# Kernel tuning notes

Measured on AMD Instinct MI355X. Metric: run time of the kernel, lower is better.

The kernel has to match this reference:

```python
import jax, jax.numpy as jnp
import numpy as np

K_DEPTH = 3
JAC_A = 1.0  # alpha (Jacobi a)
JAC_B = 1.0  # beta  (Jacobi b)


def jacobi_filter(sig, gammas):
    """Polynomial graph filter g(sigma) = sum_k gamma_k * P_k^{(a,b)}(sigma),
    Jacobi recurrence applied elementwise (Sigma is diagonal spectrum), domain [-1,1],
    fixed inner scalings (fixI=True => alphas=1)."""
    a, b = JAC_A, JAC_B
    xs = [jnp.ones_like(sig)]
    # L = 1
    coef1 = (a - b) / 2.0
    coef2 = (a + b + 2.0) / 2.0
    xs.append(coef1 * xs[0] + coef2 * sig * xs[0])
    for L in range(2, K_DEPTH + 1):
        cl = 2.0 * L * (L + a + b) * (2 * L - 2 + a + b)
        c1 = (2 * L + a + b - 1) * (2 * L + a + b) * (2 * L + a + b - 2)
        c2 = (2 * L + a + b - 1) * (a * a - b * b)
        c3 = 2.0 * (L - 1 + a) * (L - 1 + b) * (2 * L + a + b)
        xs.append((c1 / cl) * sig * xs[-1] - (c2 / cl) * xs[-1] - (c3 / cl) * xs[-2])
    basis = jnp.stack(xs, axis=0)  # [K+1, B, H, L, d]
    return jnp.einsum('k,kbhld->bhld', gammas, basis)


def setup_inputs() -> dict:
    key = jax.random.key(0)
    ks = jax.random.split(key, 7)
    B, L, Ha, Hs, d = 4, 2048, 4, 4, 64
    mk = lambda k, H: jax.random.normal(k, (B, L, H, d), dtype=jnp.float32)
    return {
        'U': mk(ks[0], Ha),
        'Sigma': mk(ks[1], Ha),
        'V': mk(ks[2], Ha),
        'values': mk(ks[3], Ha),
        'queries_softmax': mk(ks[4], Hs),
        'keys_softmax': mk(ks[5], Hs),
        'values_softmax': mk(ks[6], Hs),
        'gammas': jnp.ones((K_DEPTH + 1,), dtype=jnp.float32),
    }


def reference(U, Sigma, V, values, queries_softmax, keys_softmax, values_softmax, gammas):
    d_k = U.shape[-1]
    # ---- AGF (SVD) heads ----
    Uh = jax.nn.softmax(jnp.transpose(U, (0, 2, 1, 3)), axis=-1)        # [B,H,L,d]
    Vt = jax.nn.softmax(jnp.transpose(V, (0, 2, 3, 1)), axis=-1)        # [B,H,d,L]
    vals = jnp.transpose(values, (0, 2, 1, 3))                           # [B,H,L,d]
    sig = jax.nn.sigmoid(jnp.transpose(Sigma, (0, 2, 1, 3)))             # [B,H,L,d]
    gf = jacobi_filter(sig, gammas)                                       # [B,H,L,d]
    kv = jnp.einsum('bhdl,bhle->bhde', Vt, vals)                          # [B,H,d,d]
    out_agf = jnp.einsum('bhld,bhde->bhle', Uh * gf, kv)                  # [B,H,L,d]
    out_agf = jnp.transpose(out_agf, (0, 2, 1, 3))                        # [B,L,H,d]
    # ---- orthogonality loss ----
    eye = jnp.eye(d_k, dtype=Uh.dtype)
    sym_u = jnp.einsum('bhld,bhle->bhde', Uh, Uh) - eye
    sym_v = jnp.einsum('bhdl,bhel->bhde', Vt, Vt) - eye
    ortho_loss = jnp.mean(jnp.abs(sym_u), axis=(1, 2, 3)) + jnp.mean(jnp.abs(sym_v), axis=(1, 2, 3))
    # ---- softmax (flash) heads ----
    q = jnp.transpose(queries_softmax, (0, 2, 1, 3))
    k = jnp.transpose(keys_softmax, (0, 2, 1, 3))
    v = jnp.transpose(values_softmax, (0, 2, 1, 3))
    scores = jnp.einsum('bhld,bhsd->bhls', q, k) / jnp.sqrt(jnp.asarray(d_k, q.dtype))
    attn = jax.nn.softmax(scores, axis=-1)
    out_sm = jnp.einsum('bhls,bhsd->bhld', attn, v)
    out_sm = jnp.transpose(out_sm, (0, 2, 1, 3))                          # [B,L,H,d]
    out = jnp.concatenate([out_agf, out_sm], axis=2)                      # [B,L,2H,d]
    return out, ortho_loss
```

## Files before the change

kernel.cpp:

```cpp
#include <hip/hip_runtime.h>
#include <hip/hip_bf16.h>

#define BB 4
#define SEQ 2048
#define NH 4
#define D 64
#define NPAIR 16
#define HOUT 8
#define LOSS_BASE ((size_t)BB * SEQ * HOUT * D)

#define OFF_PART 0
#define N_PART   (4 * 16 * 3 * 4096)
#define OFF_SPART (OFF_PART + N_PART)
#define N_SPART  (16 * 32 * 64)
#define OFF_LPART (OFF_SPART + N_SPART)
#define N_LPART  (2 * 16 * 2048)
#define OFF_OPART (OFF_LPART + N_LPART)
#define N_OPART  (2 * 16 * 2048 * 64)
#define OFF_US   (OFF_OPART + N_OPART)
#define USZ ((size_t)16 * 2048 * 64)

typedef __attribute__((ext_vector_type(8))) short bf16x8;
typedef __attribute__((ext_vector_type(4))) float f32x4;
typedef __attribute__((ext_vector_type(8))) unsigned short us8;
typedef __attribute__((ext_vector_type(4))) unsigned short us4;

__device__ __forceinline__ unsigned short f2bf(float x) {
    union { float f; unsigned u; } v; v.f = x;
    unsigned r = v.u + 0x7fffu + ((v.u >> 16) & 1u);
    return (unsigned short)(r >> 16);
}
__device__ __forceinline__ float bf2f(unsigned short u) {
    union { unsigned u; float f; } v; v.u = ((unsigned)u) << 16; return v.f;
}
__device__ __forceinline__ void load16(const float* p, float* v) {
    const float4* q = (const float4*)p;
    float4 a = q[0], b = q[1], c = q[2], d = q[3];
    v[0]=a.x; v[1]=a.y; v[2]=a.z; v[3]=a.w;
    v[4]=b.x; v[5]=b.y; v[6]=b.z; v[7]=b.w;
    v[8]=c.x; v[9]=c.y; v[10]=c.z; v[11]=c.w;
    v[12]=d.x; v[13]=d.y; v[14]=d.z; v[15]=d.w;
}
__device__ __forceinline__ void wr_bf16x16(unsigned short* dst, const float* v) {
    us8 w0, w1;
#pragma unroll
    for (int i = 0; i < 8; i++) { w0[i] = f2bf(v[i]); w1[i] = f2bf(v[8 + i]); }
    *(us8*)dst = w0; *(us8*)(dst + 8) = w1;
}

__global__ __launch_bounds__(256) void prep(const float* __restrict__ U, const float* __restrict__ Vagf,
                                            const float* __restrict__ vals, const float* __restrict__ Ksm,
                                            const float* __restrict__ Vsm,
                                            float* __restrict__ ws, unsigned short* __restrict__ usb,
                                            float* __restrict__ out) {
    int lt = blockIdx.x, p = blockIdx.y;
    int b = p >> 2, h = p & 3;
    int tid = threadIdx.x;
    int r = tid >> 2;
    int c4 = tid & 3;
    int c0 = c4 * 16;
    __shared__ float T[64][68];
    unsigned short* Khi   = usb;
    unsigned short* VbfT  = usb + USZ;
    unsigned short* UhT   = usb + 2 * USZ;
    unsigned short* EhiT  = usb + 3 * USZ;
    unsigned short* EloT  = usb + 4 * USZ;
    unsigned short* valsT = usb + 5 * USZ;
    float* Spart = ws + OFF_SPART;

    const size_t gbase = ((size_t)(b * SEQ + lt * 64 + r) * NH + h) * D + c0;
    const size_t tbase = ((size_t)p * 64 + r) * 2048 + lt * 64 + c0;
    float v[16], e[16];

    load16(U + gbase, v);
    float mx = v[0];
#pragma unroll
    for (int k = 1; k < 16; k++) mx = fmaxf(mx, v[k]);
    mx = fmaxf(mx, __shfl_xor(mx, 1));
    mx = fmaxf(mx, __shfl_xor(mx, 2));
    float sm = 0.0f;
#pragma unroll
    for (int k = 0; k < 16; k++) { v[k] = __expf(v[k] - mx); sm += v[k]; }
    sm += __shfl_xor(sm, 1);
    sm += __shfl_xor(sm, 2);
    float inv = 1.0f / sm;
#pragma unroll
    for (int k = 0; k < 16; k++) T[r][c0 + k] = v[k] * inv;
    __syncthreads();
#pragma unroll
    for (int k = 0; k < 16; k++) e[k] = T[c0 + k][r];
    wr_bf16x16(UhT + tbase, e);
    __syncthreads();

    load16(Vagf + gbase, v);
#pragma unroll
    for (int k = 0; k < 16; k++) T[r][c0 + k] = __expf(v[k]);
    __syncthreads();
    float ssum = 0.0f;
#pragma unroll
    for (int k = 0; k < 16; k++) { e[k] = T[c0 + k][r]; ssum += e[k]; }
    ssum += __shfl_xor(ssum, 1);
    ssum += __shfl_xor(ssum, 2);
    if (c4 == 0) Spart[(p * 32 + lt) * 64 + r] = ssum;
    {
        us8 h0, h1, l0, l1;
#pragma unroll
        for (int i = 0; i < 8; i++) {
            unsigned short hh = f2bf(e[i]);
            h0[i] = hh; l0[i] = f2bf(e[i] - bf2f(hh));
            unsigned short h2 = f2bf(e[8 + i]);
            h1[i] = h2; l1[i] = f2bf(e[8 + i] - bf2f(h2));
        }
        *(us8*)(EhiT + tbase) = h0; *(us8*)(EhiT + tbase + 8) = h1;
        *(us8*)(EloT + tbase) = l0; *(us8*)(EloT + tbase + 8) = l1;
    }
    __syncthreads();

    load16(vals + gbase, v);
#pragma unroll
    for (int k = 0; k < 16; k++) T[r][c0 + k] = v[k];
    __syncthreads();
#pragma unroll
    for (int k = 0; k < 16; k++) e[k] = T[c0 + k][r];
    wr_bf16x16(valsT + tbase, e);
    __syncthreads();

    load16(Vsm + gbase, v);
#pragma unroll
    for (int k = 0; k < 16; k++) T[r][c0 + k] = v[k];
    __syncthreads();
#pragma unroll
    for (int k = 0; k < 16; k++) e[k] = T[c0 + k][r];
    wr_bf16x16(VbfT + tbase, e);

    load16(Ksm + gbase, v);
    wr_bf16x16(Khi + ((size_t)(p * SEQ + lt * 64 + r)) * 64 + c0, v);

    if (lt == 0 && p == 0 && tid < BB) out[LOSS_BASE + tid] = 0.0f;
}

__global__ __launch_bounds__(256) void gram(const unsigned short* __restrict__ usb,
                                            float* __restrict__ part) {
    int split = blockIdx.x, p = blockIdx.y;
    int tid = threadIdx.x;
    int w = tid >> 6, lane = tid & 63, lm = lane & 15, quad = lane >> 4;
    const unsigned short* UhT   = usb + 2 * USZ;
    const unsigned short* EhiT  = usb + 3 * USZ;
    const unsigned short* EloT  = usb + 4 * USZ;
    const unsigned short* valsT = usb + 5 * USZ;
    __shared__ __align__(16) unsigned short Ut[64 * 40], Eh[64 * 40], El[64 * 40], Vt[64 * 40];
    f32x4 su[4], sv[4], kv[4];
#pragma unroll
    for (int i = 0; i < 4; i++) { su[i] = (f32x4){0,0,0,0}; sv[i] = (f32x4){0,0,0,0}; kv[i] = (f32x4){0,0,0,0}; }
    int srow = tid >> 2;
    int sseg = (tid & 3) * 8;

    for (int step = 0; step < 16; ++step) {
        int l0 = split * 512 + step * 32;
        __syncthreads();
        size_t gb = ((size_t)p * 64 + srow) * 2048 + l0 + sseg;
        *(us8*)&Ut[srow * 40 + sseg] = *(const us8*)(UhT + gb);
        *(us8*)&Eh[srow * 40 + sseg] = *(const us8*)(EhiT + gb);
        *(us8*)&El[srow * 40 + sseg] = *(const us8*)(EloT + gb);
        *(us8*)&Vt[srow * 40 + sseg] = *(const us8*)(valsT + gb);
        __syncthreads();
        int ao = (w * 16 + lm) * 40 + quad * 8;
        bf16x8 au  = *(const bf16x8*)&Ut[ao];
        bf16x8 aeh = *(const bf16x8*)&Eh[ao];
        bf16x8 ael = *(const bf16x8*)&El[ao];
#pragma unroll
        for (int nt = 0; nt < 4; nt++) {
            int bo = (nt * 16 + lm) * 40 + quad * 8;
            bf16x8 bu  = *(const bf16x8*)&Ut[bo];
            bf16x8 beh = *(const bf16x8*)&Eh[bo];
            bf16x8 bv  = *(const bf16x8*)&Vt[bo];
            su[nt] = __builtin_amdgcn_mfma_f32_16x16x32_bf16(au,  bu,  su[nt], 0, 0, 0);
            sv[nt] = __builtin_amdgcn_mfma_f32_16x16x32_bf16(aeh, beh, sv[nt], 0, 0, 0);
            kv[nt] = __builtin_amdgcn_mfma_f32_16x16x32_bf16(aeh, bv,  kv[nt], 0, 0, 0);
            kv[nt] = __builtin_amdgcn_mfma_f32_16x16x32_bf16(ael, bv,  kv[nt], 0, 0, 0);
        }
    }
    float* dst = part + (size_t)(split * 16 + p) * 3 * 4096;
#pragma unroll
    for (int nt = 0; nt < 4; nt++)
#pragma unroll
        for (int reg = 0; reg < 4; reg++) {
            int off = (w * 16 + quad * 4 + reg) * 64 + nt * 16 + lm;
            dst[off] = su[nt][reg];
            dst[4096 + off] = sv[nt][reg];
            dst[8192 + off] = kv[nt][reg];
        }
}

__global__ __launch_bounds__(256) void agf_ortho(const float* __restrict__ U, const float* __restrict__ Sg,
                                                 const float* __restrict__ gam, const float* __restrict__ part,
                                                 const float* __restrict__ Spart, float* __restrict__ out) {
    int p = blockIdx.y;
    int tid = threadIdx.x;
    __shared__ float cis[64];
    __shared__ float red[4][64];
    {
        int d = tid & 63, grp = tid >> 6;
        float s = 0.0f;
#pragma unroll
        for (int i = 0; i < 8; i++) s += Spart[(p * 32 + grp * 8 + i) * 64 + d];
        red[grp][d] = s;
        __syncthreads();
        if (tid < 64) cis[tid] = 1.0f / (red[0][tid] + red[1][tid] + red[2][tid] + red[3][tid]);
        __syncthreads();
    }
    if (blockIdx.x == 32) {
        float s = 0.0f;
        for (int idx = tid; idx < 8192; idx += 256) {
            int g = idx >> 12, i = idx & 4095;
            float v = 0.0f;
#pragma unroll
            for (int sp = 0; sp < 4; sp++) v += part[((size_t)(sp * 16 + p) * 3 + g) * 4096 + i];
            if (g) v *= cis[i >> 6] * cis[i & 63];
            float dg = ((i >> 6) == (i & 63)) ? 1.0f : 0.0f;
            s += fabsf(v - dg);
        }
#pragma unroll
        for (int o = 32; o > 0; o >>= 1) s += __shfl_xor(s, o);
        __shared__ float r4[4];
        if ((tid & 63) == 0) r4[tid >> 6] = s;
        __syncthreads();
        if (tid == 0) atomicAdd(&out[LOSS_BASE + (p >> 2)], (r4[0] + r4[1] + r4[2] + r4[3]) * (1.0f / 16384.0f));
        return;
    }
    int lt = blockIdx.x;
    int b = p >> 2, h = p & 3;
    __shared__ __align__(16) float kvs[64][68];
    __shared__ __align__(16) float ugs[64][68];
    for (int idx = tid; idx < 4096; idx += 256) {
        float v = 0.0f;
#pragma unroll
        for (int sp = 0; sp < 4; sp++) v += part[((size_t)(sp * 16 + p) * 3 + 2) * 4096 + idx];
        kvs[idx >> 6][idx & 63] = v * cis[idx >> 6];
    }
    {
        int row = tid >> 2;
        int c16 = (tid & 3) * 16;
        size_t ibase = ((size_t)((b * SEQ + lt * 64 + row) * NH + h)) * D + c16;
        float uv[16];
        load16(U + ibase, uv);
        float mx = uv[0];
#pragma unroll
        for (int k = 1; k < 16; k++) mx = fmaxf(mx, uv[k]);
        mx = fmaxf(mx, __shfl_xor(mx, 1));
        mx = fmaxf(mx, __shfl_xor(mx, 2));
        float sm = 0.0f;
#pragma unroll
        for (int k = 0; k < 16; k++) { uv[k] = __expf(uv[k] - mx); sm += uv[k]; }
        sm += __shfl_xor(sm, 1);
        sm += __shfl_xor(sm, 2);
        float inv = 1.0f / sm;
        float sg[16];
        load16(Sg + ibase, sg);
        float g0 = gam[0], g1 = gam[1], g2 = gam[2], g3 = gam[3];
#pragma unroll
        for (int k = 0; k < 16; k++) {
            float sig = 1.0f / (1.0f + __expf(-sg[k]));
            float x1 = 2.0f * sig;
            float x2 = 1.875f * sig * x1 - 0.75f;
            float x3 = 1.8666666666666667f * sig * x2 - 0.8f * x1;
            float gf = g0 + g1 * x1 + g2 * x2 + g3 * x3;
            ugs[row][c16 + k] = uv[k] * inv * gf;
        }
    }
    __syncthreads();
    int tx = tid & 15, ty = tid >> 4;
    float acc[4][4] = {};
#pragma unroll 8
    for (int x = 0; x < 64; x++) {
        float4 kt = *(const float4*)&kvs[x][tx * 4];
        float kb[4] = {kt.x, kt.y, kt.z, kt.w};
#pragma unroll
        for (int a = 0; a < 4; a++) {
            float ua = ugs[ty * 4 + a][x];
#pragma unroll
            for (int e2 = 0; e2 < 4; e2++) acc[a][e2] = fmaf(ua, kb[e2], acc[a][e2]);
        }
    }
#pragma unroll
    for (int a = 0; a < 4; a++)
#pragma unroll
        for (int e2 = 0; e2 < 4; e2++)
            out[((size_t)(b * SEQ + lt * 64 + ty * 4 + a) * HOUT + h) * D + tx * 4 + e2] = acc[a][e2];
}

#define LSTR 72
#define FIXM 10.0f

__global__ __launch_bounds__(256, 4) void flash4(const unsigned short* __restrict__ usb,
                                                 const float* __restrict__ Q,
                                                 float* __restrict__ Opart, float* __restrict__ lpart) {
    int qt = blockIdx.x, p = blockIdx.y, half = blockIdx.z;
    int b = p >> 2, h = p & 3;
    const unsigned short* Khi  = usb;
    const unsigned short* VbfT = usb + USZ;
    __shared__ __align__(16) unsigned short Kl[64 * LSTR];
    __shared__ __align__(16) unsigned short Vl[64 * LSTR];
    __shared__ __align__(16) unsigned short Ph[4][16 * LSTR];
    const int tid = threadIdx.x;
    const int w = tid >> 6, lane = tid & 63, lm = lane & 15, quad = lane >> 4;
    const int srow = tid >> 2, sseg = (tid & 3) * 16;

    bf16x8 qhi[2], qlo[2];
    {
        int row = qt * 64 + w * 16 + lm;
        const float* qp = Q + ((size_t)(b * SEQ + row) * NH + h) * D + quad * 8;
#pragma unroll
        for (int ks = 0; ks < 2; ks++) {
            float4 a0 = *(const float4*)(qp + ks * 32);
            float4 a1 = *(const float4*)(qp + ks * 32 + 4);
            float qq[8] = {a0.x, a0.y, a0.z, a0.w, a1.x, a1.y, a1.z, a1.w};
#pragma unroll
            for (int j = 0; j < 8; j++) {
                float xs = qq[j] * 0.125f;
                unsigned short hi = f2bf(xs);
                qhi[ks][j] = (short)hi;
                qlo[ks][j] = (short)f2bf(xs - bf2f(hi));
            }
        }
    }

    float rsum = 0.0f;
    f32x4 o[4];
#pragma unroll
    for (int t = 0; t < 4; t++) o[t] = (f32x4){0.f, 0.f, 0.f, 0.f};

    us8 kr0, kr1, vr0, vr1;
    {
        int kt = half * 16;
        size_t kb = ((size_t)p * SEQ + kt * 64 + srow) * 64 + sseg;
        kr0 = *(const us8*)(Khi + kb); kr1 = *(const us8*)(Khi + kb + 8);
        size_t vb = ((size_t)p * 64 + srow) * 2048 + kt * 64 + sseg;
        vr0 = *(const us8*)(VbfT + vb); vr1 = *(const us8*)(VbfT + vb + 8);
    }

    for (int it = 0; it < 16; ++it) {
        __syncthreads();
        *(us8*)&Kl[srow * LSTR + sseg] = kr0; *(us8*)&Kl[srow * LSTR + sseg + 8] = kr1;
        *(us8*)&Vl[srow * LSTR + sseg] = vr0; *(us8*)&Vl[srow * LSTR + sseg + 8] = vr1;
        if (it < 15) {
            int kn = half * 16 + it + 1;
            size_t kb = ((size_t)p * SEQ + kn * 64 + srow) * 64 + sseg;
            kr0 = *(const us8*)(Khi + kb); kr1 = *(const us8*)(Khi + kb + 8);
            size_t vb = ((size_t)p * 64 + srow) * 2048 + kn * 64 + sseg;
            vr0 = *(const us8*)(VbfT + vb); vr1 = *(const us8*)(VbfT + vb + 8);
        }
        __syncthreads();

        f32x4 s[4];
#pragma unroll
        for (int t = 0; t < 4; t++) s[t] = (f32x4){0.f, 0.f, 0.f, 0.f};
#pragma unroll
        for (int t = 0; t < 4; t++) {
#pragma unroll
            for (int ks = 0; ks < 2; ks++) {
                bf16x8 a = *(const bf16x8*)&Kl[(t * 16 + lm) * LSTR + ks * 32 + quad * 8];
                s[t] = __builtin_amdgcn_mfma_f32_16x16x32_bf16(a, qhi[ks], s[t], 0, 0, 0);
                s[t] = __builtin_amdgcn_mfma_f32_16x16x32_bf16(a, qlo[ks], s[t], 0, 0, 0);
            }
        }

#pragma unroll
        for (int t = 0; t < 4; t++) {
            float e0 = __expf(s[t][0] - FIXM);
            float e1 = __expf(s[t][1] - FIXM);
            float e2 = __expf(s[t][2] - FIXM);
            float e3 = __expf(s[t][3] - FIXM);
            rsum += (e0 + e1) + (e2 + e3);
            union { __hip_bfloat162 h2[2]; us4 u4; } pk;
            pk.h2[0] = __float22bfloat162_rn(make_float2(e0, e1));
            pk.h2[1] = __float22bfloat162_rn(make_float2(e2, e3));
            *(us4*)&Ph[w][lm * LSTR + t * 16 + quad * 4] = pk.u4;
        }

        bf16x8 pb0 = *(const bf16x8*)&Ph[w][lm * LSTR + quad * 8];
        bf16x8 pb1 = *(const bf16x8*)&Ph[w][lm * LSTR + 32 + quad * 8];
#pragma unroll
        for (int dt = 0; dt < 4; dt++) {
            bf16x8 a0 = *(const bf16x8*)&Vl[(dt * 16 + lm) * LSTR + quad * 8];
            o[dt] = __builtin_amdgcn_mfma_f32_16x16x32_bf16(a0, pb0, o[dt], 0, 0, 0);
            bf16x8 a1 = *(const bf16x8*)&Vl[(dt * 16 + lm) * LSTR + 32 + quad * 8];
            o[dt] = __builtin_amdgcn_mfma_f32_16x16x32_bf16(a1, pb1, o[dt], 0, 0, 0);
        }
    }

    rsum += __shfl_xor(rsum, 16);
    rsum += __shfl_xor(rsum, 32);
    int row = qt * 64 + w * 16 + lm;
    size_t ob = ((size_t)(half * 16 + p) * SEQ + row) * 64;
#pragma unroll
    for (int dt = 0; dt < 4; dt++)
        *(f32x4*)(Opart + ob + dt * 16 + quad * 4) = o[dt];
    if (quad == 0) lpart[(size_t)(half * 16 + p) * SEQ + row] = rsum;
}

__global__ __launch_bounds__(256) void smerge(const float* __restrict__ Opart, const float* __restrict__ lpart,
                                              float* __restrict__ out) {
    int idx = blockIdx.x * 256 + threadIdx.x;
    int p = idx >> 15;
    int rem = idx & 32767;
    int l = rem >> 4, dq = rem & 15;
    int b = p >> 2, h = p & 3;
    size_t o0 = ((size_t)p * SEQ + l) * 64 + dq * 4;
    size_t o1 = ((size_t)(16 + p) * SEQ + l) * 64 + dq * 4;
    f32x4 a = *(const f32x4*)(Opart + o0);
    f32x4 c = *(const f32x4*)(Opart + o1);
    float inv = 1.0f / (lpart[(size_t)p * SEQ + l] + lpart[(size_t)(16 + p) * SEQ + l]);
    *(f32x4*)(out + ((size_t)(b * SEQ + l) * HOUT + 4 + h) * D + dq * 4) = (a + c) * inv;
}

extern "C" void kernel_launch(void* const* d_in, const int* in_sizes, int n_in,
                              void* d_out, int out_size, void* d_ws, size_t ws_size,
                              hipStream_t stream) {
    (void)in_sizes; (void)n_in; (void)out_size; (void)ws_size;
    const float* U    = (const float*)d_in[0];
    const float* Sg   = (const float*)d_in[1];
    const float* V    = (const float*)d_in[2];
    const float* vals = (const float*)d_in[3];
    const float* Qs   = (const float*)d_in[4];
    const float* Ks   = (const float*)d_in[5];
    const float* Vv   = (const float*)d_in[6];
    const float* gam  = (const float*)d_in[7];
    float* out = (float*)d_out;

    float* ws = (float*)d_ws;
    float* part  = ws + OFF_PART;
    float* Spart = ws + OFF_SPART;
    float* lpart = ws + OFF_LPART;
    float* Opart = ws + OFF_OPART;
    unsigned short* usb = (unsigned short*)(ws + OFF_US);

    prep<<<dim3(32, 16), 256, 0, stream>>>(U, V, vals, Ks, Vv, ws, usb, out);
    gram<<<dim3(4, 16), 256, 0, stream>>>(usb, part);
    agf_ortho<<<dim3(33, 16), 256, 0, stream>>>(U, Sg, gam, part, Spart, out);
    flash4<<<dim3(32, 16, 2), 256, 0, stream>>>(usb, Qs, Opart, lpart);
    smerge<<<(NPAIR * SEQ * 16) / 256, 256, 0, stream>>>(Opart, lpart, out);
}
```

Before: 180.3 us.

## Fuse gram and flash into one launch, merge AGF and softmax epilogues

Merges the gram (Gram/kv partial) kernel and the flash-attention kernel into one launch with a block-index split, so the two independent stages share the GPU. Gram work is split into 8 chunks instead of 4 to create more blocks. Flash is restructured so each wave holds its K/V fragments in registers with a register prefetch instead of staging them through shared memory, and each wave covers a key slice across all 64 queries with per-wave row sums. The AGF output and softmax merge kernels are combined into one launch. This cuts launch count and serial dependencies, at the cost of larger partial buffers and an extra reduction over per-wave sums.

Result: no change. 180.7 us (+0.2%).

```diff
diff --git a/kernel.cpp b/kernel.cpp
--- a/kernel.cpp
+++ b/kernel.cpp
@@ -10,11 +10,11 @@
 #define LOSS_BASE ((size_t)BB * SEQ * HOUT * D)
 
 #define OFF_PART 0
-#define N_PART   (4 * 16 * 3 * 4096)
+#define N_PART   (8 * 16 * 3 * 4096)
 #define OFF_SPART (OFF_PART + N_PART)
 #define N_SPART  (16 * 32 * 64)
 #define OFF_LPART (OFF_SPART + N_SPART)
-#define N_LPART  (2 * 16 * 2048)
+#define N_LPART  (2 * 16 * 4 * 2048)
 #define OFF_OPART (OFF_LPART + N_LPART)
 #define N_OPART  (2 * 16 * 2048 * 64)
 #define OFF_US   (OFF_OPART + N_OPART)
@@ -139,64 +139,191 @@
     if (lt == 0 && p == 0 && tid < BB) out[LOSS_BASE + tid] = 0.0f;
 }
 
-__global__ __launch_bounds__(256) void gram(const unsigned short* __restrict__ usb,
-                                            float* __restrict__ part) {
-    int split = blockIdx.x, p = blockIdx.y;
-    int tid = threadIdx.x;
-    int w = tid >> 6, lane = tid & 63, lm = lane & 15, quad = lane >> 4;
-    const unsigned short* UhT   = usb + 2 * USZ;
-    const unsigned short* EhiT  = usb + 3 * USZ;
-    const unsigned short* EloT  = usb + 4 * USZ;
-    const unsigned short* valsT = usb + 5 * USZ;
-    __shared__ __align__(16) unsigned short Ut[64 * 40], Eh[64 * 40], El[64 * 40], Vt[64 * 40];
-    f32x4 su[4], sv[4], kv[4];
-#pragma unroll
-    for (int i = 0; i < 4; i++) { su[i] = (f32x4){0,0,0,0}; sv[i] = (f32x4){0,0,0,0}; kv[i] = (f32x4){0,0,0,0}; }
-    int srow = tid >> 2;
-    int sseg = (tid & 3) * 8;
-
-    for (int step = 0; step < 16; ++step) {
-        int l0 = split * 512 + step * 32;
-        __syncthreads();
-        size_t gb = ((size_t)p * 64 + srow) * 2048 + l0 + sseg;
-        *(us8*)&Ut[srow * 40 + sseg] = *(const us8*)(UhT + gb);
-        *(us8*)&Eh[srow * 40 + sseg] = *(const us8*)(EhiT + gb);
-        *(us8*)&El[srow * 40 + sseg] = *(const us8*)(EloT + gb);
-        *(us8*)&Vt[srow * 40 + sseg] = *(const us8*)(valsT + gb);
-        __syncthreads();
-        int ao = (w * 16 + lm) * 40 + quad * 8;
-        bf16x8 au  = *(const bf16x8*)&Ut[ao];
-        bf16x8 aeh = *(const bf16x8*)&Eh[ao];
-        bf16x8 ael = *(const bf16x8*)&El[ao];
-#pragma unroll
-        for (int nt = 0; nt < 4; nt++) {
-            int bo = (nt * 16 + lm) * 40 + quad * 8;
-            bf16x8 bu  = *(const bf16x8*)&Ut[bo];
-            bf16x8 beh = *(const bf16x8*)&Eh[bo];
-            bf16x8 bv  = *(const bf16x8*)&Vt[bo];
-            su[nt] = __builtin_amdgcn_mfma_f32_16x16x32_bf16(au,  bu,  su[nt], 0, 0, 0);
-            sv[nt] = __builtin_amdgcn_mfma_f32_16x16x32_bf16(aeh, beh, sv[nt], 0, 0, 0);
-            kv[nt] = __builtin_amdgcn_mfma_f32_16x16x32_bf16(aeh, bv,  kv[nt], 0, 0, 0);
-            kv[nt] = __builtin_amdgcn_mfma_f32_16x16x32_bf16(ael, bv,  kv[nt], 0, 0, 0);
-        }
-    }
-    float* dst = part + (size_t)(split * 16 + p) * 3 * 4096;
-#pragma unroll
-    for (int nt = 0; nt < 4; nt++)
-#pragma unroll
-        for (int reg = 0; reg < 4; reg++) {
-            int off = (w * 16 + quad * 4 + reg) * 64 + nt * 16 + lm;
-            dst[off] = su[nt][reg];
-            dst[4096 + off] = sv[nt][reg];
-            dst[8192 + off] = kv[nt][reg];
-        }
-}
-
-__global__ __launch_bounds__(256) void agf_ortho(const float* __restrict__ U, const float* __restrict__ Sg,
-                                                 const float* __restrict__ gam, const float* __restrict__ part,
-                                                 const float* __restrict__ Spart, float* __restrict__ out) {
-    int p = blockIdx.y;
-    int tid = threadIdx.x;
+#define PSTR 72
+#define FIXM 10.0f
+
+__global__ __launch_bounds__(256, 3) void mid(const unsigned short* __restrict__ usb,
+                                              const float* __restrict__ Q,
+                                              float* __restrict__ part,
+                                              float* __restrict__ Opart, float* __restrict__ lpart) {
+    __shared__ __align__(16) unsigned char smem[20480];
+    const int bid = blockIdx.x;
+    const int tid = threadIdx.x;
+    const int w = tid >> 6, lane = tid & 63, lm = lane & 15, quad = lane >> 4;
+
+    if (bid < 1024) {
+        int qt = bid & 31, p = (bid >> 5) & 15, half = bid >> 9;
+        int b = p >> 2, h = p & 3;
+        const unsigned short* Khi  = usb;
+        const unsigned short* VbfT = usb + USZ;
+        unsigned short* Ph = (unsigned short*)smem;
+
+        bf16x8 qhi[4][2], qlo[4][2];
+#pragma unroll
+        for (int nq = 0; nq < 4; nq++) {
+            const float* qp = Q + ((size_t)(b * SEQ + qt * 64 + nq * 16 + lm) * NH + h) * D + quad * 8;
+#pragma unroll
+            for (int ks = 0; ks < 2; ks++) {
+                float4 a0 = *(const float4*)(qp + ks * 32);
+                float4 a1 = *(const float4*)(qp + ks * 32 + 4);
+                float qq[8] = {a0.x, a0.y, a0.z, a0.w, a1.x, a1.y, a1.z, a1.w};
+#pragma unroll
+                for (int j = 0; j < 8; j++) {
+                    float xs = qq[j] * 0.125f;
+                    unsigned short hi = f2bf(xs);
+                    qhi[nq][ks][j] = (short)hi;
+                    qlo[nq][ks][j] = (short)f2bf(xs - bf2f(hi));
+                }
+            }
+        }
+
+        float rsum[4] = {0.f, 0.f, 0.f, 0.f};
+        f32x4 o[4];
+#pragma unroll
+        for (int t = 0; t < 4; t++) o[t] = (f32x4){0.f, 0.f, 0.f, 0.f};
+
+        const size_t kbase = ((size_t)p * SEQ + (size_t)half * 1024 + w * 16 + lm) * 64 + quad * 8;
+        const size_t vbase = ((size_t)p * 64 + w * 16 + lm) * 2048 + (size_t)half * 1024 + quad * 8;
+        bf16x8 kf[2], vf[2], kf2[2], vf2[2];
+#pragma unroll
+        for (int ks = 0; ks < 2; ks++) {
+            kf[ks] = *(const bf16x8*)(Khi + kbase + ks * 32);
+            vf[ks] = *(const bf16x8*)(VbfT + vbase + ks * 32);
+        }
+
+        for (int it = 0; it < 16; ++it) {
+            f32x4 s[4];
+#pragma unroll
+            for (int t = 0; t < 4; t++) s[t] = (f32x4){0.f, 0.f, 0.f, 0.f};
+#pragma unroll
+            for (int ks = 0; ks < 2; ks++)
+#pragma unroll
+                for (int nq = 0; nq < 4; nq++) {
+                    s[nq] = __builtin_amdgcn_mfma_f32_16x16x32_bf16(kf[ks], qhi[nq][ks], s[nq], 0, 0, 0);
+                    s[nq] = __builtin_amdgcn_mfma_f32_16x16x32_bf16(kf[ks], qlo[nq][ks], s[nq], 0, 0, 0);
+                }
+            if (it < 15) {
+#pragma unroll
+                for (int ks = 0; ks < 2; ks++) {
+                    kf2[ks] = *(const bf16x8*)(Khi + kbase + (it + 1) * 64ull * 64 + ks * 32);
+                    vf2[ks] = *(const bf16x8*)(VbfT + vbase + (it + 1) * 64 + ks * 32);
+                }
+            }
+#pragma unroll
+            for (int nq = 0; nq < 4; nq++) {
+                us4 pk;
+#pragma unroll
+                for (int r = 0; r < 4; r++) {
+                    float e = __expf(s[nq][r] - FIXM);
+                    rsum[nq] += e;
+                    pk[r] = f2bf(e);
+                }
+                *(us4*)&Ph[(nq * 16 + lm) * PSTR + w * 16 + quad * 4] = pk;
+            }
+            __syncthreads();
+
+#pragma unroll
+            for (int ks = 0; ks < 2; ks++)
+#pragma unroll
+                for (int nq = 0; nq < 4; nq++) {
+                    bf16x8 pf = *(const bf16x8*)&Ph[(nq * 16 + lm) * PSTR + ks * 32 + quad * 8];
+                    o[nq] = __builtin_amdgcn_mfma_f32_16x16x32_bf16(vf[ks], pf, o[nq], 0, 0, 0);
+                }
+            __syncthreads();
+#pragma unroll
+            for (int ks = 0; ks < 2; ks++) { kf[ks] = kf2[ks]; vf[ks] = vf2[ks]; }
+        }
+
+#pragma unroll
+        for (int nq = 0; nq < 4; nq++) {
+            float rs = rsum[nq];
+            rs += __shfl_xor(rs, 16);
+            rs += __shfl_xor(rs, 32);
+            int row = qt * 64 + nq * 16 + lm;
+            *(f32x4*)(Opart + ((size_t)(half * 16 + p) * SEQ + row) * 64 + w * 16 + quad * 4) = o[nq];
+            if (quad == 0)
+                lpart[((size_t)(half * 16 + p) * 4 + w) * SEQ + row] = rs;
+        }
+    } else {
+        int j = bid - 1024;
+        int split = j >> 4, p = j & 15;
+        const unsigned short* UhT   = usb + 2 * USZ;
+        const unsigned short* EhiT  = usb + 3 * USZ;
+        const unsigned short* EloT  = usb + 4 * USZ;
+        const unsigned short* valsT = usb + 5 * USZ;
+        unsigned short* Ut = (unsigned short*)smem;
+        unsigned short* Eh = Ut + 64 * 40;
+        unsigned short* El = Eh + 64 * 40;
+        unsigned short* Vt = El + 64 * 40;
+        f32x4 su[4], sv[4], kv[4];
+#pragma unroll
+        for (int i = 0; i < 4; i++) { su[i] = (f32x4){0,0,0,0}; sv[i] = (f32x4){0,0,0,0}; kv[i] = (f32x4){0,0,0,0}; }
+        int srow = tid >> 2;
+        int sseg = (tid & 3) * 8;
+
+        for (int step = 0; step < 8; ++step) {
+            int l0 = split * 256 + step * 32;
+            __syncthreads();
+            size_t gb = ((size_t)p * 64 + srow) * 2048 + l0 + sseg;
+            *(us8*)&Ut[srow * 40 + sseg] = *(const us8*)(UhT + gb);
+            *(us8*)&Eh[srow * 40 + sseg] = *(const us8*)(EhiT + gb);
+            *(us8*)&El[srow * 40 + sseg] = *(const us8*)(EloT + gb);
+            *(us8*)&Vt[srow * 40 + sseg] = *(const us8*)(valsT + gb);
+            __syncthreads();
+            int ao = (w * 16 + lm) * 40 + quad * 8;
+            bf16x8 au  = *(const bf16x8*)&Ut[ao];
+            bf16x8 aeh = *(const bf16x8*)&Eh[ao];
+            bf16x8 ael = *(const bf16x8*)&El[ao];
+#pragma unroll
+            for (int nt = 0; nt < 4; nt++) {
+                int bo = (nt * 16 + lm) * 40 + quad * 8;
+                bf16x8 bu  = *(const bf16x8*)&Ut[bo];
+                bf16x8 beh = *(const bf16x8*)&Eh[bo];
+                bf16x8 bv  = *(const bf16x8*)&Vt[bo];
+                su[nt] = __builtin_amdgcn_mfma_f32_16x16x32_bf16(au,  bu,  su[nt], 0, 0, 0);
+                sv[nt] = __builtin_amdgcn_mfma_f32_16x16x32_bf16(aeh, beh, sv[nt], 0, 0, 0);
+                kv[nt] = __builtin_amdgcn_mfma_f32_16x16x32_bf16(aeh, bv,  kv[nt], 0, 0, 0);
+                kv[nt] = __builtin_amdgcn_mfma_f32_16x16x32_bf16(ael, bv,  kv[nt], 0, 0, 0);
+            }
+        }
+        float* dst = part + (size_t)(split * 16 + p) * 3 * 4096;
+#pragma unroll
+        for (int nt = 0; nt < 4; nt++)
+#pragma unroll
+            for (int reg = 0; reg < 4; reg++) {
+                int off = (w * 16 + quad * 4 + reg) * 64 + nt * 16 + lm;
+                dst[off] = su[nt][reg];
+                dst[4096 + off] = sv[nt][reg];
+                dst[8192 + off] = kv[nt][reg];
+            }
+    }
+}
+
+__global__ __launch_bounds__(256) void post(const float* __restrict__ U, const float* __restrict__ Sg,
+                                            const float* __restrict__ gam, const float* __restrict__ part,
+                                            const float* __restrict__ Spart, const float* __restrict__ Opart,
+                                            const float* __restrict__ lpart, float* __restrict__ out) {
+    const int bid = blockIdx.x;
+    const int tid = threadIdx.x;
+    if (bid < 2048) {
+        int idx = bid * 256 + tid;
+        int p = idx >> 15;
+        int rem = idx & 32767;
+        int l = rem >> 4, dq = rem & 15;
+        int b = p >> 2, h = p & 3;
+        f32x4 a = *(const f32x4*)(Opart + ((size_t)p * SEQ + l) * 64 + dq * 4);
+        f32x4 c = *(const f32x4*)(Opart + ((size_t)(16 + p) * SEQ + l) * 64 + dq * 4);
+        float den = 0.0f;
+#pragma unroll
+        for (int hf = 0; hf < 2; hf++)
+#pragma unroll
+            for (int wv = 0; wv < 4; wv++)
+                den += lpart[((size_t)(hf * 16 + p) * 4 + wv) * SEQ + l];
+        *(f32x4*)(out + ((size_t)(b * SEQ + l) * HOUT + 4 + h) * D + dq * 4) = (a + c) * (1.0f / den);
+        return;
+    }
+    int j = bid - 2048;
+    int p = j / 33, lt = j % 33;
     __shared__ float cis[64];
     __shared__ float red[4][64];
     {
@@ -209,13 +336,13 @@
         if (tid < 64) cis[tid] = 1.0f / (red[0][tid] + red[1][tid] + red[2][tid] + red[3][tid]);
         __syncthreads();
     }
-    if (blockIdx.x == 32) {
+    if (lt == 32) {
         float s = 0.0f;
         for (int idx = tid; idx < 8192; idx += 256) {
             int g = idx >> 12, i = idx & 4095;
             float v = 0.0f;
 #pragma unroll
-            for (int sp = 0; sp < 4; sp++) v += part[((size_t)(sp * 16 + p) * 3 + g) * 4096 + i];
+            for (int sp = 0; sp < 8; sp++) v += part[((size_t)(sp * 16 + p) * 3 + g) * 4096 + i];
             if (g) v *= cis[i >> 6] * cis[i & 63];
             float dg = ((i >> 6) == (i & 63)) ? 1.0f : 0.0f;
             s += fabsf(v - dg);
@@ -228,14 +355,13 @@
         if (tid == 0) atomicAdd(&out[LOSS_BASE + (p >> 2)], (r4[0] + r4[1] + r4[2] + r4[3]) * (1.0f / 16384.0f));
         return;
     }
-    int lt = blockIdx.x;
     int b = p >> 2, h = p & 3;
     __shared__ __align__(16) float kvs[64][68];
     __shared__ __align__(16) float ugs[64][68];
     for (int idx = tid; idx < 4096; idx += 256) {
         float v = 0.0f;
 #pragma unroll
-        for (int sp = 0; sp < 4; sp++) v += part[((size_t)(sp * 16 + p) * 3 + 2) * 4096 + idx];
+        for (int sp = 0; sp < 8; sp++) v += part[((size_t)(sp * 16 + p) * 3 + 2) * 4096 + idx];
         kvs[idx >> 6][idx & 63] = v * cis[idx >> 6];
     }
     {
@@ -287,131 +413,6 @@
 #pragma unroll
         for (int e2 = 0; e2 < 4; e2++)
             out[((size_t)(b * SEQ + lt * 64 + ty * 4 + a) * HOUT + h) * D + tx * 4 + e2] = acc[a][e2];
-}
-
-#define LSTR 72
-#define FIXM 10.0f
-
-__global__ __launch_bounds__(256, 4) void flash4(const unsigned short* __restrict__ usb,
-                                                 const float* __restrict__ Q,
-                                                 float* __restrict__ Opart, float* __restrict__ lpart) {
-    int qt = blockIdx.x, p = blockIdx.y, half = blockIdx.z;
-    int b = p >> 2, h = p & 3;
-    const unsigned short* Khi  = usb;
-    const unsigned short* VbfT = usb + USZ;
-    __shared__ __align__(16) unsigned short Kl[64 * LSTR];
-    __shared__ __align__(16) unsigned short Vl[64 * LSTR];
-    __shared__ __align__(16) unsigned short Ph[4][16 * LSTR];
-    const int tid = threadIdx.x;
-    const int w = tid >> 6, lane = tid & 63, lm = lane & 15, quad = lane >> 4;
-    const int srow = tid >> 2, sseg = (tid & 3) * 16;
-
-    bf16x8 qhi[2], qlo[2];
-    {
-        int row = qt * 64 + w * 16 + lm;
-        const float* qp = Q + ((size_t)(b * SEQ + row) * NH + h) * D + quad * 8;
-#pragma unroll
-        for (int ks = 0; ks < 2; ks++) {
-            float4 a0 = *(const float4*)(qp + ks * 32);
-            float4 a1 = *(const float4*)(qp + ks * 32 + 4);
-            float qq[8] = {a0.x, a0.y, a0.z, a0.w, a1.x, a1.y, a1.z, a1.w};
-#pragma unroll
-            for (int j = 0; j < 8; j++) {
-                float xs = qq[j] * 0.125f;
-                unsigned short hi = f2bf(xs);
-                qhi[ks][j] = (short)hi;
-                qlo[ks][j] = (short)f2bf(xs - bf2f(hi));
-            }
-        }
-    }
-
-    float rsum = 0.0f;
-    f32x4 o[4];
-#pragma unroll
-    for (int t = 0; t < 4; t++) o[t] = (f32x4){0.f, 0.f, 0.f, 0.f};
-
-    us8 kr0, kr1, vr0, vr1;
-    {
-        int kt = half * 16;
-        size_t kb = ((size_t)p * SEQ + kt * 64 + srow) * 64 + sseg;
-        kr0 = *(const us8*)(Khi + kb); kr1 = *(const us8*)(Khi + kb + 8);
-        size_t vb = ((size_t)p * 64 + srow) * 2048 + kt * 64 + sseg;
-        vr0 = *(const us8*)(VbfT + vb); vr1 = *(const us8*)(VbfT + vb + 8);
-    }
-
-    for (int it = 0; it < 16; ++it) {
-        __syncthreads();
-        *(us8*)&Kl[srow * LSTR + sseg] = kr0; *(us8*)&Kl[srow * LSTR + sseg + 8] = kr1;
-        *(us8*)&Vl[srow * LSTR + sseg] = vr0; *(us8*)&Vl[srow * LSTR + sseg + 8] = vr1;
-        if (it < 15) {
-            int kn = half * 16 + it + 1;
-            size_t kb = ((size_t)p * SEQ + kn * 64 + srow) * 64 + sseg;
-            kr0 = *(const us8*)(Khi + kb); kr1 = *(const us8*)(Khi + kb + 8);
-            size_t vb = ((size_t)p * 64 + srow) * 2048 + kn * 64 + sseg;
-            vr0 = *(const us8*)(VbfT + vb); vr1 = *(const us8*)(VbfT + vb + 8);
-        }
-        __syncthreads();
-
-        f32x4 s[4];
-#pragma unroll
-        for (int t = 0; t < 4; t++) s[t] = (f32x4){0.f, 0.f, 0.f, 0.f};
-#pragma unroll
-        for (int t = 0; t < 4; t++) {
-#pragma unroll
-            for (int ks = 0; ks < 2; ks++) {
-                bf16x8 a = *(const bf16x8*)&Kl[(t * 16 + lm) * LSTR + ks * 32 + quad * 8];
-                s[t] = __builtin_amdgcn_mfma_f32_16x16x32_bf16(a, qhi[ks], s[t], 0, 0, 0);
-                s[t] = __builtin_amdgcn_mfma_f32_16x16x32_bf16(a, qlo[ks], s[t], 0, 0, 0);
-            }
-        }
-
-#pragma unroll
-        for (int t = 0; t < 4; t++) {
-            float e0 = __expf(s[t][0] - FIXM);
-            float e1 = __expf(s[t][1] - FIXM);
-            float e2 = __expf(s[t][2] - FIXM);
-            float e3 = __expf(s[t][3] - FIXM);
-            rsum += (e0 + e1) + (e2 + e3);
-            union { __hip_bfloat162 h2[2]; us4 u4; } pk;
-            pk.h2[0] = __float22bfloat162_rn(make_float2(e0, e1));
-            pk.h2[1] = __float22bfloat162_rn(make_float2(e2, e3));
-            *(us4*)&Ph[w][lm * LSTR + t * 16 + quad * 4] = pk.u4;
-        }
-
-        bf16x8 pb0 = *(const bf16x8*)&Ph[w][lm * LSTR + quad * 8];
-        bf16x8 pb1 = *(const bf16x8*)&Ph[w][lm * LSTR + 32 + quad * 8];
-#pragma unroll
-        for (int dt = 0; dt < 4; dt++) {
-            bf16x8 a0 = *(const bf16x8*)&Vl[(dt * 16 + lm) * LSTR + quad * 8];
-            o[dt] = __builtin_amdgcn_mfma_f32_16x16x32_bf16(a0, pb0, o[dt], 0, 0, 0);
-            bf16x8 a1 = *(const bf16x8*)&Vl[(dt * 16 + lm) * LSTR + 32 + quad * 8];
-            o[dt] = __builtin_amdgcn_mfma_f32_16x16x32_bf16(a1, pb1, o[dt], 0, 0, 0);
-        }
-    }
-
-    rsum += __shfl_xor(rsum, 16);
-    rsum += __shfl_xor(rsum, 32);
-    int row = qt * 64 + w * 16 + lm;
-    size_t ob = ((size_t)(half * 16 + p) * SEQ + row) * 64;
-#pragma unroll
-    for (int dt = 0; dt < 4; dt++)
-        *(f32x4*)(Opart + ob + dt * 16 + quad * 4) = o[dt];
-    if (quad == 0) lpart[(size_t)(half * 16 + p) * SEQ + row] = rsum;
-}
-
-__global__ __launch_bounds__(256) void smerge(const float* __restrict__ Opart, const float* __restrict__ lpart,
-                                              float* __restrict__ out) {
-    int idx = blockIdx.x * 256 + threadIdx.x;
-    int p = idx >> 15;
-    int rem = idx & 32767;
-    int l = rem >> 4, dq = rem & 15;
-    int b = p >> 2, h = p & 3;
-    size_t o0 = ((size_t)p * SEQ + l) * 64 + dq * 4;
-    size_t o1 = ((size_t)(16 + p) * SEQ + l) * 64 + dq * 4;
-    f32x4 a = *(const f32x4*)(Opart + o0);
-    f32x4 c = *(const f32x4*)(Opart + o1);
-    float inv = 1.0f / (lpart[(size_t)p * SEQ + l] + lpart[(size_t)(16 + p) * SEQ + l]);
-    *(f32x4*)(out + ((size_t)(b * SEQ + l) * HOUT + 4 + h) * D + dq * 4) = (a + c) * inv;
 }
 
 extern "C" void kernel_launch(void* const* d_in, const int* in_sizes, int n_in,
@@ -436,8 +437,6 @@
     unsigned short* usb = (unsigned short*)(ws + OFF_US);
 
     prep<<<dim3(32, 16), 256, 0, stream>>>(U, V, vals, Ks, Vv, ws, usb, out);
-    gram<<<dim3(4, 16), 256, 0, stream>>>(usb, part);
-    agf_ortho<<<dim3(33, 16), 256, 0, stream>>>(U, Sg, gam, part, Spart, out);
-    flash4<<<dim3(32, 16, 2), 256, 0, stream>>>(usb, Qs, Opart, lpart);
-    smerge<<<(NPAIR * SEQ * 16) / 256, 256, 0, stream>>>(Opart, lpart, out);
-}
+    mid<<<1152, 256, 0, stream>>>(usb, Qs, part, Opart, lpart);
+    post<<<2576, 256, 0, stream>>>(U, Sg, gam, part, Spart, Opart, lpart, out);
+}
```
